# Performance work log

Hardware: AMD Instinct MI355X
Metric: run time of the kernel (lower is better)

Reference implementation:

```python
import jax, jax.numpy as jnp
import numpy as np

B, L, N, DM = 32, 12, 883, 64
DSP, DTP, H, HID, HOR = 128, 128, 4, 64, 12
E_SPA = 14128
ENC_LAYERS = 3
HIDDEN = 5 * HID  # 2*embed + node + tid + diw = 320


def _gat(x, es, et, W, a_s, a_d, bias, edge_att=None):
    # GATConv-style attention with optional per-edge info-bottleneck mask (gat_ib)
    n = x.shape[0]
    h = (x @ W).reshape(n, H, -1)            # [n,H,Dh]
    sc_s = (h * a_s).sum(-1)                 # [n,H]
    sc_d = (h * a_d).sum(-1)
    al = jax.nn.leaky_relu(sc_s[es] + sc_d[et], 0.2)   # [E,H]
    al = al - jax.ops.segment_max(al, et, num_segments=n)[et]
    ex = jnp.exp(al)
    a = ex / jax.ops.segment_sum(ex, et, num_segments=n)[et]
    if edge_att is not None:
        a = a * edge_att[:, None]
    out = jax.ops.segment_sum(a[..., None] * h[es], et, num_segments=n)
    return out.reshape(n, -1) + bias


def _gsat(x, ei, gat_p, ext_p):
    # GSAT: embed -> extractor MLP on edge endpoint pairs -> sigmoid edge att -> masked conv
    es, et = ei[0], ei[1]
    emb = _gat(x, es, et, *gat_p)
    w1, b1, w2, b2, w3, b3 = ext_p
    f = jnp.concatenate([emb[es], emb[et]], axis=-1)
    logit = (jax.nn.relu(jax.nn.relu(f @ w1 + b1) @ w2 + b2) @ w3 + b3)[:, 0]
    att = jax.nn.sigmoid(logit)  # eval-mode (no concrete-relaxation sampling)
    return _gat(x, es, et, *gat_p, edge_att=att)


def setup_inputs():
    key = jax.random.key(0)
    ks = iter(jax.random.split(key, 80))
    def nrm(shape, s=0.02):
        return jax.random.normal(next(ks), shape, jnp.float32) * s
    hist = jax.random.normal(next(ks), (B, L, N, 3), jnp.float32)
    tid = jax.random.randint(next(ks), (B, L, N), 0, 288).astype(jnp.float32)
    diw = jax.random.randint(next(ks), (B, L, N), 0, 7).astype(jnp.float32)
    hist = hist.at[..., 1].set(tid).at[..., 2].set(diw)
    ei_spa = jax.random.randint(next(ks), (2, E_SPA), 0, N).astype(jnp.int32)
    g = jnp.arange(L, dtype=jnp.int32)
    ei_temp = jnp.stack([jnp.repeat(g, L), jnp.tile(g, L)])  # dense lag x lag temporal graph
    inp = dict(history_data=hist, edge_idx_spa=ei_spa, edge_idx_temp=ei_temp)
    inp.update(
        node_emb=nrm((N, HID)), tid_emb=nrm((288, HID)), diw_emb=nrm((7, HID)),
        start_w=nrm((3, DM)), start_b=jnp.zeros((DM,), jnp.float32),
        ts_w=nrm((DM * L, HID)), ts_b=jnp.zeros((HID,), jnp.float32),
        tr_spat_w=nrm((L * DM, DSP)), tr_spat_b=jnp.zeros((DSP,), jnp.float32),
        inv_spat_w=nrm((DSP, L * DM)), inv_spat_b=jnp.zeros((L * DM,), jnp.float32),
        tr_temp_w=nrm((N * DM, DTP)), tr_temp_b=jnp.zeros((DTP,), jnp.float32),
        inv_temp_w=nrm((DTP, N * DM)), inv_temp_b=jnp.zeros((N * DM,), jnp.float32),
        gat_sp_w=nrm((DSP, DSP)), gat_sp_asrc=nrm((H, DSP // H)), gat_sp_adst=nrm((H, DSP // H)), gat_sp_bias=jnp.zeros((DSP,), jnp.float32),
        ext_sp_w1=nrm((2 * DSP, 4 * DSP)), ext_sp_b1=jnp.zeros((4 * DSP,), jnp.float32),
        ext_sp_w2=nrm((4 * DSP, DSP)), ext_sp_b2=jnp.zeros((DSP,), jnp.float32),
        ext_sp_w3=nrm((DSP, 1)), ext_sp_b3=jnp.zeros((1,), jnp.float32),
        gat_tp_w=nrm((DTP, DTP)), gat_tp_asrc=nrm((H, DTP // H)), gat_tp_adst=nrm((H, DTP // H)), gat_tp_bias=jnp.zeros((DTP,), jnp.float32),
        ext_tp_w1=nrm((2 * DTP, 4 * DTP)), ext_tp_b1=jnp.zeros((4 * DTP,), jnp.float32),
        ext_tp_w2=nrm((4 * DTP, DTP)), ext_tp_b2=jnp.zeros((DTP,), jnp.float32),
        ext_tp_w3=nrm((DTP, 1)), ext_tp_b3=jnp.zeros((1,), jnp.float32),
        enc_w1=nrm((ENC_LAYERS, HIDDEN, HIDDEN)), enc_b1=jnp.zeros((ENC_LAYERS, HIDDEN), jnp.float32),
        enc_w2=nrm((ENC_LAYERS, HIDDEN, HIDDEN)), enc_b2=jnp.zeros((ENC_LAYERS, HIDDEN), jnp.float32),
        reg_w=nrm((HIDDEN, HOR)), reg_b=jnp.zeros((HOR,), jnp.float32),
    )
    return inp


def reference(history_data, edge_idx_spa, edge_idx_temp, node_emb, tid_emb, diw_emb,
              start_w, start_b, ts_w, ts_b,
              tr_spat_w, tr_spat_b, inv_spat_w, inv_spat_b,
              tr_temp_w, tr_temp_b, inv_temp_w, inv_temp_b,
              gat_sp_w, gat_sp_asrc, gat_sp_adst, gat_sp_bias,
              ext_sp_w1, ext_sp_b1, ext_sp_w2, ext_sp_b2, ext_sp_w3, ext_sp_b3,
              gat_tp_w, gat_tp_asrc, gat_tp_adst, gat_tp_bias,
              ext_tp_w1, ext_tp_b1, ext_tp_w2, ext_tp_b2, ext_tp_w3, ext_tp_b3,
              enc_w1, enc_b1, enc_w2, enc_b2, reg_w, reg_b):
    b, l, n = history_data.shape[:3]
    tid = jax.lax.stop_gradient(history_data[:, -1, :, 1]).astype(jnp.int32)
    diw = jax.lax.stop_gradient(history_data[:, -1, :, 2]).astype(jnp.int32)
    X = history_data[..., :3] @ start_w + start_b           # [B,L,N,DM]
    res = X.transpose(0, 2, 1, 3).reshape(b, n, l * DM)      # [B,N,L*DM]
    ts_res = res @ ts_w + ts_b                               # conv1x1 over nodes == per-node linear
    gp_sp = (gat_sp_w, gat_sp_asrc, gat_sp_adst, gat_sp_bias)
    ep_sp = (ext_sp_w1, ext_sp_b1, ext_sp_w2, ext_sp_b2, ext_sp_w3, ext_sp_b3)
    gp_tp = (gat_tp_w, gat_tp_asrc, gat_tp_adst, gat_tp_bias)
    ep_tp = (ext_tp_w1, ext_tp_b1, ext_tp_w2, ext_tp_b2, ext_tp_w3, ext_tp_b3)
    # batch_st_gsat: per-sample spatial GSAT then temporal GSAT (vmapped instead of Python loop)
    spa_in = res @ tr_spat_w + tr_spat_b                     # [B,N,DSP]
    spa_out = jax.vmap(lambda xx: _gsat(xx, edge_idx_spa, gp_sp, ep_sp))(spa_in)
    spa_back = (spa_out @ inv_spat_w + inv_spat_b).reshape(b, n, l, DM).transpose(0, 2, 1, 3)
    temp_in = spa_back.reshape(b, l, n * DM) @ tr_temp_w + tr_temp_b   # [B,L,DTP]
    temp_out = jax.vmap(lambda xx: _gsat(xx, edge_idx_temp, gp_tp, ep_tp))(temp_in)
    temp_back = (temp_out @ inv_temp_w + inv_temp_b).reshape(b, l, n, DM)
    ts_temp = temp_back.transpose(0, 2, 1, 3).reshape(b, n, l * DM) @ ts_w + ts_b
    hid = jnp.concatenate([
        ts_res, ts_temp,
        jnp.broadcast_to(node_emb, (b, n, HID)),
        tid_emb[tid], diw_emb[diw],
    ], axis=-1)                                              # [B,N,320]
    for i in range(ENC_LAYERS):  # MLP_res: x + fc2(relu(fc1(x)))
        hid = hid + jax.nn.relu(hid @ enc_w1[i] + enc_b1[i]) @ enc_w2[i] + enc_b2[i]
    pred = hid @ reg_w + reg_b                               # [B,N,HOR]
    return pred.transpose(0, 2, 1)[..., None]                # [B,HOR,N,1]
```

## Files before the change

kernel.cpp:

```cpp
#include <hip/hip_runtime.h>
#include <hip/hip_bf16.h>
#include <cstdint>
#include <cstddef>

#define B_   32
#define L_   12
#define N_   883
#define DM_  64
#define E_SP 14128
#define E_TP 144
#define NT_  12
#define RBN  28256
#define RBL  384
#define LDM  768
#define NDM  56512

static inline int cdiv_h(int a, int b){ return (a+b-1)/b; }

__device__ __forceinline__ ushort f2bf(float f){
    unsigned u = __float_as_uint(f);
    unsigned lsb = (u >> 16) & 1u;
    u += 0x7fffu + lsb;
    return (ushort)(u >> 16);
}
__device__ __forceinline__ float bf2f(ushort h){
    return __uint_as_float(((unsigned)h) << 16);
}
__device__ __forceinline__ ushort f2h(float f){
    _Float16 h = (_Float16)f;
    ushort r; __builtin_memcpy(&r, &h, 2);
    return r;
}

typedef __bf16 bf16x8 __attribute__((ext_vector_type(8)));
typedef _Float16 f16x8 __attribute__((ext_vector_type(8)));
typedef _Float16 f16x2 __attribute__((ext_vector_type(2)));
typedef float  f32x4  __attribute__((ext_vector_type(4)));
typedef short  s16x2  __attribute__((ext_vector_type(2)));
union BF8 { bf16x8 v; ushort u[8]; unsigned w[4]; int4 i; };
union HF8 { f16x8 v; ushort u[8]; unsigned w[4]; int4 i; };

__device__ __forceinline__ unsigned pkrelu(unsigned x){
    s16x2 v;
    __builtin_memcpy(&v, &x, 4);
    s16x2 z = 0;
    v = __builtin_elementwise_max(v, z);
    unsigned r;
    __builtin_memcpy(&r, &v, 4);
    return r;
}
__device__ __forceinline__ unsigned pkaddh(unsigned x, unsigned y){
    f16x2 a, b;
    __builtin_memcpy(&a, &x, 4);
    __builtin_memcpy(&b, &y, 4);
    a = a + b;
    unsigned r;
    __builtin_memcpy(&r, &a, 4);
    return r;
}

__global__ void k_res(const float* __restrict__ hist, const float* __restrict__ sw,
                      const float* __restrict__ sb, ushort* __restrict__ resHi,
                      ushort* __restrict__ resLo)
{
    int idx = blockIdx.x*256 + threadIdx.x;
    if (idx >= RBN*LDM) return;
    int r = idx / LDM, col = idx - r*LDM;
    int b = r / N_, n = r - b*N_;
    int l = col >> 6, d = col & 63;
    const float* hp = hist + ((size_t)(b*L_ + l)*N_ + n)*3;
    float v = hp[0]*sw[d] + hp[1]*sw[64+d] + hp[2]*sw[128+d] + sb[d];
    ushort hi = f2bf(v);
    resHi[idx] = hi;
    resLo[idx] = f2bf(v - bf2f(hi));
}

template<int CT, int AMODE, int EPI, bool RELU, bool RES>
__launch_bounds__(256)
__global__ void mgemm(const ushort* __restrict__ A, const ushort* __restrict__ WT,
                      const float* __restrict__ bias, float* __restrict__ resF,
                      void* __restrict__ outP, int M, int N, int K)
{
    const int t = threadIdx.x, wv = t >> 6, l = t & 63;
    const int lr = l & 15, lk = l >> 4;
    const int row0 = blockIdx.y*64 + wv*16;
    const int col0 = blockIdx.x * (CT*16);
    int arr = row0 + lr; if (arr >= M) arr = M-1;
    int ab = 0, an = 0;
    if (AMODE == 1) { ab = arr / N_; an = arr - ab*N_; }
    const ushort* ap = A + (size_t)arr*K + lk*8;
    f32x4 acc[CT] = {};
    for (int k0 = 0; k0 < K; k0 += 32) {
        BF8 af;
        if (AMODE == 0) af.i = *(const int4*)(ap + k0);
        else {
            int k = k0 + lk*8; int ll = k >> 6, d = k & 63;
            af.i = *(const int4*)(A + ((size_t)(ab*L_ + ll))*NDM + (size_t)an*64 + d);
        }
        #pragma unroll
        for (int ct = 0; ct < CT; ++ct) {
            BF8 bf; bf.i = *(const int4*)&WT[(size_t)(col0 + ct*16 + lr)*K + k0 + lk*8];
            acc[ct] = __builtin_amdgcn_mfma_f32_16x16x32_bf16(af.v, bf.v, acc[ct], 0, 0, 0);
        }
    }
    #pragma unroll
    for (int ct = 0; ct < CT; ++ct) {
        int c = col0 + ct*16 + lr;
        float bv = 0.f;
        if (EPI == 2) { if (bias && c < 12) bv = bias[c]; }
        else if (bias) bv = bias[c];
        #pragma unroll
        for (int g = 0; g < 4; ++g) {
            int r = row0 + lk*4 + g;
            if (r >= M) continue;
            float v = acc[ct][g] + bv;
            if (RELU) v = fmaxf(v, 0.f);
            if (RES) {
                v += resF[(size_t)r*N + c];
                resF[(size_t)r*N + c] = v;
            }
            if (EPI == 0) {
                ((ushort*)outP)[(size_t)r*N + c] = f2bf(v);
            } else if (EPI == 1) {
                ((float*)outP)[(size_t)r*N + c] = v;
            } else if (EPI == 2) {
                if (c < 12) {
                    int b = r / N_, n = r - (r/N_)*N_;
                    ((float*)outP)[((size_t)(b*L_ + c))*N_ + n] = v;
                }
            } else {
                int b = r / N_, n = r - (r/N_)*N_;
                ((ushort*)outP)[((size_t)(b*L_ + (c>>6)))*NDM + (size_t)n*64 + (c&63)] = f2bf(v);
            }
        }
    }
}

template<int RT, int CT, int EPI, bool RELU, bool RES>
__launch_bounds__(256)
__global__ void mgemm_rt(const ushort* __restrict__ A, const ushort* __restrict__ WT,
                         const float* __restrict__ bias, float* __restrict__ resF,
                         void* __restrict__ outP, int M, int N, int K)
{
    const int t = threadIdx.x, wv = t >> 6, l = t & 63;
    const int lr = l & 15, lk = l >> 4;
    const int rowbase = blockIdx.y*(4*RT*16) + wv*(RT*16);
    const int col0 = blockIdx.x * (CT*16);
    const ushort* ap[RT];
    #pragma unroll
    for (int rt = 0; rt < RT; ++rt) {
        int arr = rowbase + rt*16 + lr; if (arr >= M) arr = M-1;
        ap[rt] = A + (size_t)arr*K + lk*8;
    }
    f32x4 acc[RT][CT] = {};
    for (int k0 = 0; k0 < K; k0 += 32) {
        BF8 af[RT];
        #pragma unroll
        for (int rt = 0; rt < RT; ++rt) af[rt].i = *(const int4*)(ap[rt] + k0);
        #pragma unroll
        for (int ct = 0; ct < CT; ++ct) {
            BF8 bf; bf.i = *(const int4*)&WT[(size_t)(col0 + ct*16 + lr)*K + k0 + lk*8];
            #pragma unroll
            for (int rt = 0; rt < RT; ++rt)
                acc[rt][ct] = __builtin_amdgcn_mfma_f32_16x16x32_bf16(af[rt].v, bf.v,
                                                                     acc[rt][ct], 0, 0, 0);
        }
    }
    #pragma unroll
    for (int rt = 0; rt < RT; ++rt)
        #pragma unroll
        for (int ct = 0; ct < CT; ++ct) {
            int c = col0 + ct*16 + lr;
            float bv = bias ? bias[c] : 0.f;
            #pragma unroll
            for (int g = 0; g < 4; ++g) {
                int r = rowbase + rt*16 + lk*4 + g;
                if (r >= M) continue;
                float v = acc[rt][ct][g] + bv;
                if (RELU) v = fmaxf(v, 0.f);
                if (RES) {
                    v += resF[(size_t)r*N + c];
                    resF[(size_t)r*N + c] = v;
                }
                if (EPI == 0) {
                    ((ushort*)outP)[(size_t)r*N + c] = f2bf(v);
                } else if (EPI == 1) {
                    ((float*)outP)[(size_t)r*N + c] = v;
                } else if (EPI == 4) {
                    ((ushort*)outP)[(size_t)r*N + c] = f2h(v);
                } else {
                    int b = r / N_, n = r - (r/N_)*N_;
                    ((ushort*)outP)[((size_t)(b*L_ + (c>>6)))*NDM + (size_t)n*64 + (c&63)] = f2bf(v);
                }
            }
        }
}

template<int CT>
__launch_bounds__(256)
__global__ void mgemm_hl(const ushort* __restrict__ Ahi, const ushort* __restrict__ Alo,
                         const ushort* __restrict__ WThi, const ushort* __restrict__ WTlo,
                         const float* __restrict__ bias, float* __restrict__ outF,
                         int M, int N, int K)
{
    const int t = threadIdx.x, wv = t >> 6, l = t & 63;
    const int lr = l & 15, lk = l >> 4;
    const int row0 = blockIdx.y*64 + wv*16;
    const int col0 = blockIdx.x * (CT*16);
    int arr = row0 + lr; if (arr >= M) arr = M-1;
    const ushort* aph = Ahi + (size_t)arr*K + lk*8;
    const ushort* apl = Alo + (size_t)arr*K + lk*8;
    f32x4 acc[CT] = {};
    for (int k0 = 0; k0 < K; k0 += 32) {
        BF8 ah, al_;
        ah.i  = *(const int4*)(aph + k0);
        al_.i = *(const int4*)(apl + k0);
        #pragma unroll
        for (int ct = 0; ct < CT; ++ct) {
            size_t wo = (size_t)(col0 + ct*16 + lr)*K + k0 + lk*8;
            BF8 bh, bl;
            bh.i = *(const int4*)&WThi[wo];
            bl.i = *(const int4*)&WTlo[wo];
            acc[ct] = __builtin_amdgcn_mfma_f32_16x16x32_bf16(ah.v,  bh.v, acc[ct], 0, 0, 0);
            acc[ct] = __builtin_amdgcn_mfma_f32_16x16x32_bf16(al_.v, bh.v, acc[ct], 0, 0, 0);
            acc[ct] = __builtin_amdgcn_mfma_f32_16x16x32_bf16(ah.v,  bl.v, acc[ct], 0, 0, 0);
        }
    }
    #pragma unroll
    for (int ct = 0; ct < CT; ++ct) {
        int c = col0 + ct*16 + lr;
        float bv = bias ? bias[c] : 0.f;
        #pragma unroll
        for (int g = 0; g < 4; ++g) {
            int r = row0 + lk*4 + g;
            if (r >= M) continue;
            outF[(size_t)r*N + c] = acc[ct][g] + bv;
        }
    }
}

#define TCH 1024
__launch_bounds__(256)
__global__ void temp_in_mfma(const ushort* __restrict__ AT, const ushort* __restrict__ WtT,
                             float* __restrict__ out)
{
    const int t = threadIdx.x, wv = t >> 6, l = t & 63;
    const int lr = l & 15, lk = l >> 4;
    const int row0 = blockIdx.y * 96;
    const int c0 = wv * 32;
    const int k0b = blockIdx.x * TCH;
    const int kend = (k0b + TCH < NDM) ? (k0b + TCH) : NDM;
    f32x4 acc[6][2] = {};
    for (int k0 = k0b; k0 < kend; k0 += 32) {
        BF8 b0, b1;
        b0.i = *(const int4*)&WtT[(size_t)(c0 + lr)*NDM + k0 + lk*8];
        b1.i = *(const int4*)&WtT[(size_t)(c0 + 16 + lr)*NDM + k0 + lk*8];
        #pragma unroll
        for (int m = 0; m < 6; ++m) {
            BF8 af; af.i = *(const int4*)&AT[(size_t)(row0 + m*16 + lr)*NDM + k0 + lk*8];
            acc[m][0] = __builtin_amdgcn_mfma_f32_16x16x32_bf16(af.v, b0.v, acc[m][0], 0, 0, 0);
            acc[m][1] = __builtin_amdgcn_mfma_f32_16x16x32_bf16(af.v, b1.v, acc[m][1], 0, 0, 0);
        }
    }
    #pragma unroll
    for (int m = 0; m < 6; ++m)
        #pragma unroll
        for (int ct = 0; ct < 2; ++ct) {
            int c = c0 + ct*16 + lr;
            #pragma unroll
            for (int g = 0; g < 4; ++g) {
                int r = row0 + m*16 + lk*4 + g;
                atomicAdd(&out[(size_t)r*128 + c], acc[m][ct][g]);
            }
        }
}

__global__ void k_sc(const ushort* __restrict__ h, const float* __restrict__ as_,
                     const float* __restrict__ ad_, float* __restrict__ scs,
                     float* __restrict__ scd, int R)
{
    int r = blockIdx.x*256 + threadIdx.x;
    if (r >= R) return;
    const ushort* hr = h + (size_t)r*128;
    #pragma unroll
    for (int hh = 0; hh < 4; ++hh) {
        float ss = 0.f, sd = 0.f;
        #pragma unroll
        for (int k = 0; k < 32; ++k) {
            float hv = bf2f(hr[hh*32 + k]);
            ss += hv*as_[hh*32+k];
            sd += hv*ad_[hh*32+k];
        }
        scs[(size_t)r*4+hh] = ss;
        scd[(size_t)r*4+hh] = sd;
    }
}

__global__ void k_attE(const float* __restrict__ scs, const float* __restrict__ scd,
                       const int* __restrict__ ei, int E, int NN,
                       float* __restrict__ a_buf, float* __restrict__ nsum)
{
    int idx = blockIdx.x*256 + threadIdx.x;
    if (idx >= B_*E) return;
    int b = idx / E, e = idx - b*E;
    int s = ei[e], tg = ei[E+e];
    const float* ps = scs + (size_t)(b*NN+s)*4;
    const float* pd = scd + (size_t)(b*NN+tg)*4;
    float* ns = nsum + (size_t)(b*NN+tg)*4;
    float* pa = a_buf + (size_t)idx*4;
    #pragma unroll
    for (int hh = 0; hh < 4; ++hh) {
        float al = ps[hh] + pd[hh];
        al = al > 0.f ? al : 0.2f*al;
        float ex = expf(al);
        pa[hh] = ex;
        atomicAdd(ns + hh, ex);
    }
}

__global__ void k_count(const int* __restrict__ ei, int E, int* __restrict__ counts){
    int e = blockIdx.x*256 + threadIdx.x;
    if (e < E) atomicAdd(&counts[ei[E + e]], 1);
}
__global__ void k_scan(const int* __restrict__ counts, int* __restrict__ off,
                       int* __restrict__ cur, int n)
{
    __shared__ int s[1024];
    int t = threadIdx.x;
    int v0 = (t < n) ? counts[t] : 0;
    s[t] = v0;
    __syncthreads();
    for (int o = 1; o < 1024; o <<= 1) {
        int v = (t >= o) ? s[t-o] : 0;
        __syncthreads();
        s[t] += v;
        __syncthreads();
    }
    if (t < n) {
        off[t+1] = s[t];
        cur[t] = s[t] - v0;
        if (t == 0) off[0] = 0;
    }
}
__global__ void k_fill(const int* __restrict__ ei, int E, int* __restrict__ cur,
                       int* __restrict__ lst){
    int e = blockIdx.x*256 + threadIdx.x;
    if (e < E) {
        int pos = atomicAdd(&cur[ei[E+e]], 1);
        lst[pos] = e;
    }
}

template<bool USE_ATT>
__global__ void k_gather(const ushort* __restrict__ h, const float* __restrict__ a_buf,
                         const float* __restrict__ nsum, const float* __restrict__ att,
                         const int* __restrict__ ei, const int* __restrict__ off,
                         const int* __restrict__ lst, const float* __restrict__ bias,
                         ushort* __restrict__ out, int E, int NN)
{
    int bn = blockIdx.x*4 + (threadIdx.x >> 6);
    int b = bn / NN, n = bn - b*NN;
    int lane = threadIdx.x & 63;
    int c0 = lane*2;
    int hh = lane >> 4;
    float rn = 1.f / nsum[(size_t)bn*4 + hh];
    int o0 = off[n], o1 = off[n+1];
    float ax = 0.f, ay = 0.f;
    for (int i = o0; i < o1; ++i) {
        int e = lst[i];
        float a = a_buf[((size_t)b*E + e)*4 + hh] * rn;
        if (USE_ATT) a *= att[(size_t)b*E + e];
        int s = ei[e];
        unsigned hv = *(const unsigned*)&h[((size_t)b*NN + s)*128 + c0];
        ax += a * __uint_as_float(hv << 16);
        ay += a * __uint_as_float(hv & 0xffff0000u);
    }
    ushort2 o2;
    o2.x = f2bf(ax + bias[c0]);
    o2.y = f2bf(ay + bias[c0+1]);
    *(ushort2*)&out[(size_t)bn*128 + c0] = o2;
}

__global__ void k_prepW2(const float* __restrict__ W2, ushort* __restrict__ W2T)
{
    int idx = blockIdx.x*256 + threadIdx.x;
    if (idx >= 512*128) return;
    int k = idx >> 7, c = idx & 127;
    W2T[(size_t)c*512 + k] = f2h(W2[idx]);
}
__global__ void k_prepT(const float* __restrict__ W, ushort* __restrict__ WT, int K, int N)
{
    int idx = blockIdx.x*256 + threadIdx.x;
    if (idx >= K*N) return;
    int k = idx / N, c = idx - k*N;
    WT[(size_t)c*K + k] = f2bf(W[idx]);
}
__global__ void k_prepT_hl(const float* __restrict__ W, ushort* __restrict__ WThi,
                           ushort* __restrict__ WTlo, int K, int N)
{
    int idx = blockIdx.x*256 + threadIdx.x;
    if (idx >= K*N) return;
    int k = idx / N, c = idx - k*N;
    float v = W[idx];
    ushort hi = f2bf(v);
    WThi[(size_t)c*K + k] = hi;
    WTlo[(size_t)c*K + k] = f2bf(v - bf2f(hi));
}
__global__ void k_prepWtT(const float* __restrict__ W, ushort* __restrict__ WT)
{
    __shared__ ushort tile[128][129];
    int k0 = blockIdx.x * 128;
    int t = threadIdx.x;
    for (int i = t; i < 128*128; i += 256) {
        int k = i >> 7, c = i & 127;
        int kk = k0 + k;
        tile[c][k] = (kk < NDM) ? f2bf(W[(size_t)kk*128 + c]) : (ushort)0;
    }
    __syncthreads();
    for (int i = t; i < 128*128; i += 256) {
        int c = i >> 7, k = i & 127;
        int kk = k0 + k;
        if (kk < NDM) WT[(size_t)c*NDM + kk] = tile[c][k];
    }
}
__global__ void k_prepT_big(const float* __restrict__ W, ushort* __restrict__ WT)
{
    __shared__ float tile[128][65];
    int c0 = blockIdx.x * 64;
    int t = threadIdx.x;
    for (int i = t; i < 128*64; i += 256) {
        int k = i >> 6, ci = i & 63;
        tile[k][ci] = W[(size_t)k*NDM + c0 + ci];
    }
    __syncthreads();
    for (int i = t; i < 64*128; i += 256) {
        int ci = i >> 7, k = i & 127;
        WT[(size_t)(c0 + ci)*128 + k] = f2bf(tile[k][ci]);
    }
}
__global__ void k_bcat(const float* __restrict__ b1, float* __restrict__ dst){
    int i = blockIdx.x*256 + threadIdx.x;
    if (i < 1024) dst[i] = (i < 512) ? b1[i] : 0.f;
}

template<bool SWZ>
__launch_bounds__(256, 3)
__global__ void ext2_mfma(const ushort* __restrict__ PQ, const ushort* __restrict__ W2T,
                          const float* __restrict__ b2, const float* __restrict__ w3,
                          const float* __restrict__ b3p, const int* __restrict__ ei,
                          const int* __restrict__ lst,
                          float* __restrict__ att, int E, int NN, int nblk)
{
    __shared__ ushort Bs[2][128*40];
    int bid = blockIdx.x;
    if (SWZ) {
        bid = (blockIdx.x & 7) * (gridDim.x >> 3) + (blockIdx.x >> 3);
        if (bid >= nblk) bid = nblk - 1;
    }
    const int t = threadIdx.x;
    const int wv = t >> 6, l = t & 63;
    const int lr = l & 15, lk = l >> 4;

    const ushort* pr[2]; const ushort* qr[2];
    int row0[2];
    #pragma unroll
    for (int rt = 0; rt < 2; ++rt) {
        row0[rt] = bid*128 + wv*32 + rt*16;
        int r = row0[rt] + lr;
        int b = (int)((unsigned)r / (unsigned)E), i = r - b*E;
        int e = lst[i];
        pr[rt] = PQ + ((size_t)b*NN + ei[e])*1024 + lk*8;
        qr[rt] = PQ + ((size_t)b*NN + ei[E+e])*1024 + 512 + lk*8;
    }
    const int sc = t >> 1, sh = (t & 1) * 16;
    const ushort* wsrc = W2T + (size_t)sc*512 + sh;
    ushort* wd0 = &Bs[0][sc*40 + sh];
    ushort* wd1 = &Bs[1][sc*40 + sh];

    {
        int4 a0 = *(const int4*)(wsrc);
        int4 a1 = *(const int4*)(wsrc + 8);
        *(int4*)wd0 = a0;
        *(int4*)(wd0 + 8) = a1;
    }
    HF8 pu[2], qu[2];
    #pragma unroll
    for (int rt = 0; rt < 2; ++rt) {
        pu[rt].i = *(const int4*)(pr[rt]);
        qu[rt].i = *(const int4*)(qr[rt]);
    }
    int4 bnA = *(const int4*)(wsrc + 32);
    int4 bnB = *(const int4*)(wsrc + 40);
    __syncthreads();

    f32x4 acc[2][8] = {};
    for (int kc = 0; kc < 16; ++kc) {
        const int cb = kc & 1;
        HF8 af[2];
        #pragma unroll
        for (int rt = 0; rt < 2; ++rt)
            #pragma unroll
            for (int j = 0; j < 4; ++j)
                af[rt].w[j] = pkrelu(pkaddh(pu[rt].w[j], qu[rt].w[j]));
        {
            int ka = (kc+1 < 15) ? kc+1 : 15;
            #pragma unroll
            for (int rt = 0; rt < 2; ++rt) {
                pu[rt].i = *(const int4*)(pr[rt] + ka*32);
                qu[rt].i = *(const int4*)(qr[rt] + ka*32);
            }
        }
        __builtin_amdgcn_s_setprio(1);
        #pragma unroll
        for (int ct = 0; ct < 8; ++ct) {
            HF8 bfm;
            bfm.v = *(const f16x8*)&Bs[cb][(ct*16 + lr)*40 + lk*8];
            #pragma unroll
            for (int rt = 0; rt < 2; ++rt)
                acc[rt][ct] = __builtin_amdgcn_mfma_f32_16x16x32_f16(af[rt].v, bfm.v,
                                                                    acc[rt][ct], 0, 0, 0);
        }
        __builtin_amdgcn_s_setprio(0);
        if (kc < 15) {
            ushort* wd = cb ? wd0 : wd1;
            *(int4*)wd = bnA;
            *(int4*)(wd + 8) = bnB;
        }
        {
            int kb = (kc+2 < 15) ? kc+2 : 15;
            bnA = *(const int4*)(wsrc + kb*32);
            bnB = *(const int4*)(wsrc + kb*32 + 8);
        }
        __syncthreads();
    }
    float b3 = b3p[0];
    #pragma unroll
    for (int rt = 0; rt < 2; ++rt) {
        float part[4] = {0.f,0.f,0.f,0.f};
        #pragma unroll
        for (int ct = 0; ct < 8; ++ct) {
            int c = ct*16 + lr;
            float b2v = b2[c], w3v = w3[c];
            #pragma unroll
            for (int g = 0; g < 4; ++g)
                part[g] += fmaxf(acc[rt][ct][g] + b2v, 0.f) * w3v;
        }
        #pragma unroll
        for (int m = 1; m < 16; m <<= 1)
            #pragma unroll
            for (int g = 0; g < 4; ++g)
                part[g] += __shfl_xor(part[g], m, 64);
        if (lr == 0) {
            #pragma unroll
            for (int g = 0; g < 4; ++g) {
                int rr = row0[rt] + lk*4 + g;
                int b = (int)((unsigned)rr / (unsigned)E), i = rr - b*E;
                int e = lst[i];
                att[(size_t)b*E + e] = 1.f/(1.f + expf(-(part[g] + b3)));
            }
        }
    }
}

__global__ void k_bias_fill(float* __restrict__ dst, const float* __restrict__ bias, int n){
    int i = blockIdx.x*256 + threadIdx.x;
    if (i < n) dst[i] = bias[i & 127];
}
__global__ void k_f2b(const float* __restrict__ src, ushort* __restrict__ dst, int n){
    int i = blockIdx.x*256 + threadIdx.x;
    if (i < n) dst[i] = f2bf(src[i]);
}

__global__ void k_hid(const float* __restrict__ ts_res, const float* __restrict__ ts_temp,
                      const float* __restrict__ node_emb, const float* __restrict__ tid_emb,
                      const float* __restrict__ diw_emb, const float* __restrict__ hist,
                      float* __restrict__ hid, ushort* __restrict__ hidB)
{
    int idx = blockIdx.x*256 + threadIdx.x;
    if (idx >= RBN*320) return;
    int r = idx / 320, c = idx - r*320;
    int b = r / N_, n = r - b*N_;
    float v;
    if (c < 64)        v = ts_res[(size_t)r*64 + c];
    else if (c < 128)  v = ts_temp[(size_t)r*64 + (c-64)];
    else if (c < 192)  v = node_emb[(size_t)n*64 + (c-128)];
    else if (c < 256) {
        int tid = (int)hist[((size_t)(b*L_ + (L_-1))*N_ + n)*3 + 1];
        v = tid_emb[(size_t)tid*64 + (c-192)];
    } else {
        int diw = (int)hist[((size_t)(b*L_ + (L_-1))*N_ + n)*3 + 2];
        v = diw_emb[(size_t)diw*64 + (c-256)];
    }
    hid[idx] = v;
    hidB[idx] = f2bf(v);
}

extern "C" void kernel_launch(void* const* d_in, const int* in_sizes, int n_in,
                              void* d_out, int out_size, void* d_ws, size_t ws_size,
                              hipStream_t stream)
{
    (void)in_sizes; (void)n_in; (void)out_size; (void)ws_size;
    const float* hist      = (const float*)d_in[0];
    const int*   ei_sp     = (const int*)  d_in[1];
    const int*   ei_tp     = (const int*)  d_in[2];
    const float* node_emb  = (const float*)d_in[3];
    const float* tid_emb   = (const float*)d_in[4];
    const float* diw_emb   = (const float*)d_in[5];
    const float* start_w   = (const float*)d_in[6];
    const float* start_b   = (const float*)d_in[7];
    const float* ts_w      = (const float*)d_in[8];
    const float* ts_b      = (const float*)d_in[9];
    const float* tr_spat_w = (const float*)d_in[10];
    const float* tr_spat_b = (const float*)d_in[11];
    const float* inv_spat_w= (const float*)d_in[12];
    const float* inv_spat_b= (const float*)d_in[13];
    const float* tr_temp_w = (const float*)d_in[14];
    const float* tr_temp_b = (const float*)d_in[15];
    const float* inv_temp_w= (const float*)d_in[16];
    const float* inv_temp_b= (const float*)d_in[17];
    const float* gat_sp_w  = (const float*)d_in[18];
    const float* gat_sp_as = (const float*)d_in[19];
    const float* gat_sp_ad = (const float*)d_in[20];
    const float* gat_sp_b  = (const float*)d_in[21];
    const float* ext_sp_w1 = (const float*)d_in[22];
    const float* ext_sp_b1 = (const float*)d_in[23];
    const float* ext_sp_w2 = (const float*)d_in[24];
    const float* ext_sp_b2 = (const float*)d_in[25];
    const float* ext_sp_w3 = (const float*)d_in[26];
    const float* ext_sp_b3 = (const float*)d_in[27];
    const float* gat_tp_w  = (const float*)d_in[28];
    const float* gat_tp_as = (const float*)d_in[29];
    const float* gat_tp_ad = (const float*)d_in[30];
    const float* gat_tp_b  = (const float*)d_in[31];
    const float* ext_tp_w1 = (const float*)d_in[32];
    const float* ext_tp_b1 = (const float*)d_in[33];
    const float* ext_tp_w2 = (const float*)d_in[34];
    const float* ext_tp_b2 = (const float*)d_in[35];
    const float* ext_tp_w3 = (const float*)d_in[36];
    const float* ext_tp_b3 = (const float*)d_in[37];
    const float* enc_w1    = (const float*)d_in[38];
    const float* enc_b1    = (const float*)d_in[39];
    const float* enc_w2    = (const float*)d_in[40];
    const float* enc_b2    = (const float*)d_in[41];
    const float* reg_w     = (const float*)d_in[42];
    const float* reg_b     = (const float*)d_in[43];
    float* out = (float*)d_out;

    size_t o = 0;
    char* wsb = (char*)d_ws;
    auto allocB = [&](size_t bytes) -> void* {
        void* p = wsb + o;
        o += (bytes + 255) & ~(size_t)255;
        return p;
    };
    void* bufA = allocB((size_t)RBN*768*2);
    void* bufB = allocB((size_t)RBN*768*2);
    void* bufC = allocB((size_t)RBN*512*2);
    void* bufD = allocB((size_t)RBN*320*2);
    float*  ts_res  = (float*)allocB((size_t)RBN*64*4);
    ushort* spaB    = (ushort*)allocB((size_t)RBN*128*2);
    ushort* hB      = (ushort*)allocB((size_t)RBN*128*2);
    float*  sc_s    = (float*)allocB((size_t)RBN*4*4);
    float*  sc_d    = (float*)allocB((size_t)RBN*4*4);
    float*  nsum    = (float*)allocB((size_t)RBN*4*4);
    float*  a_buf   = (float*)allocB((size_t)B_*E_SP*4*4);
    float*  att     = (float*)allocB((size_t)B_*E_SP*4);
    ushort* embB    = (ushort*)allocB((size_t)RBN*128*2);
    int*    csr     = (int*)allocB(17024*4);
    float*  temp_in = (float*)allocB((size_t)RBL*128*4);
    ushort* tempB   = (ushort*)allocB((size_t)RBL*128*2);
    ushort* toutB   = (ushort*)allocB((size_t)RBL*128*2);
    ushort* PQ_t    = (ushort*)allocB((size_t)RBL*1024*2);
    float*  ts_temp = (float*)allocB((size_t)RBN*64*4);
    ushort* W2T_sp  = (ushort*)allocB(512*128*2);
    ushort* W2T_tp  = (ushort*)allocB(512*128*2);
    ushort* WtT     = (ushort*)allocB((size_t)128*NDM*2);
    ushort* itWT    = (ushort*)allocB((size_t)NDM*128*2);
    ushort* tspWT   = (ushort*)allocB(128*768*2);
    ushort* ispWT   = (ushort*)allocB(768*128*2);
    ushort* gspWT   = (ushort*)allocB(128*128*2);
    ushort* gtpWT   = (ushort*)allocB(128*128*2);
    ushort* w1catT_sp = (ushort*)allocB((size_t)1024*128*2);
    ushort* w1catT_tp = (ushort*)allocB((size_t)1024*128*2);
    float*  b1cat_sp  = (float*)allocB(1024*4);
    float*  b1cat_tp  = (float*)allocB(1024*4);
    ushort* w1T_enc = (ushort*)allocB((size_t)3*320*320*2);
    ushort* w2T_enc = (ushort*)allocB((size_t)3*320*320*2);
    ushort* tswT_hi = (ushort*)allocB(64*768*2);
    ushort* tswT_lo = (ushort*)allocB(64*768*2);
    ushort* reg_wT  = (ushort*)allocB(16*320*2);

    ushort* resHi = (ushort*)bufA;
    ushort* resLo = (ushort*)bufB;
    ushort* AT    = (ushort*)bufA;
    float*  hid   = (float*)bufA;
    ushort* PQ_sp = (ushort*)bufB;
    ushort* tback = (ushort*)bufB;
    ushort* hidB  = (ushort*)bufC;
    ushort* R1b   = (ushort*)bufD;

    int* counts_sp = csr;
    int* off_sp    = csr + 883;
    int* cur_sp    = csr + 1767;
    int* list_sp   = csr + 2650;
    int* counts_tp = csr + 16778;
    int* off_tp    = csr + 16790;
    int* cur_tp    = csr + 16803;
    int* list_tp   = csr + 16815;

    hipMemsetAsync(counts_sp, 0, 883*4, stream);
    k_count<<<cdiv_h(E_SP,256),256,0,stream>>>(ei_sp, E_SP, counts_sp);
    k_scan<<<1,1024,0,stream>>>(counts_sp, off_sp, cur_sp, 883);
    k_fill<<<cdiv_h(E_SP,256),256,0,stream>>>(ei_sp, E_SP, cur_sp, list_sp);
    hipMemsetAsync(counts_tp, 0, 12*4, stream);
    k_count<<<1,256,0,stream>>>(ei_tp, E_TP, counts_tp);
    k_scan<<<1,1024,0,stream>>>(counts_tp, off_tp, cur_tp, 12);
    k_fill<<<1,256,0,stream>>>(ei_tp, E_TP, cur_tp, list_tp);
    k_prepW2<<<cdiv_h(512*128,256),256,0,stream>>>(ext_sp_w2, W2T_sp);
    k_prepW2<<<cdiv_h(512*128,256),256,0,stream>>>(ext_tp_w2, W2T_tp);
    k_prepWtT<<<cdiv_h(NDM,128),256,0,stream>>>(tr_temp_w, WtT);
    k_prepT_big<<<NDM/64,256,0,stream>>>(inv_temp_w, itWT);
    k_prepT<<<cdiv_h(768*128,256),256,0,stream>>>(tr_spat_w, tspWT, 768, 128);
    k_prepT<<<cdiv_h(128*768,256),256,0,stream>>>(inv_spat_w, ispWT, 128, 768);
    k_prepT<<<cdiv_h(128*128,256),256,0,stream>>>(gat_sp_w, gspWT, 128, 128);
    k_prepT<<<cdiv_h(128*128,256),256,0,stream>>>(gat_tp_w, gtpWT, 128, 128);
    k_prepT<<<cdiv_h(128*512,256),256,0,stream>>>(ext_sp_w1,           w1catT_sp,           128, 512);
    k_prepT<<<cdiv_h(128*512,256),256,0,stream>>>(ext_sp_w1 + 128*512, w1catT_sp + 512*128, 128, 512);
    k_prepT<<<cdiv_h(128*512,256),256,0,stream>>>(ext_tp_w1,           w1catT_tp,           128, 512);
    k_prepT<<<cdiv_h(128*512,256),256,0,stream>>>(ext_tp_w1 + 128*512, w1catT_tp + 512*128, 128, 512);
    k_bcat<<<4,256,0,stream>>>(ext_sp_b1, b1cat_sp);
    k_bcat<<<4,256,0,stream>>>(ext_tp_b1, b1cat_tp);
    for (int i = 0; i < 3; ++i) {
        k_prepT<<<cdiv_h(320*320,256),256,0,stream>>>(enc_w1 + (size_t)i*320*320, w1T_enc + (size_t)i*320*320, 320, 320);
        k_prepT<<<cdiv_h(320*320,256),256,0,stream>>>(enc_w2 + (size_t)i*320*320, w2T_enc + (size_t)i*320*320, 320, 320);
    }
    k_prepT_hl<<<cdiv_h(768*64,256),256,0,stream>>>(ts_w, tswT_hi, tswT_lo, 768, 64);
    hipMemsetAsync(reg_wT, 0, 16*320*2, stream);
    k_prepT<<<cdiv_h(320*12,256),256,0,stream>>>(reg_w, reg_wT, 320, 12);

    k_res<<<cdiv_h(RBN*LDM,256),256,0,stream>>>(hist, start_w, start_b, resHi, resLo);
    mgemm_hl<4><<<dim3(1,442),256,0,stream>>>(resHi, resLo, tswT_hi, tswT_lo, ts_b, ts_res,
                                              RBN, 64, LDM);
    mgemm_rt<2,4,0,false,false><<<dim3(2,221),256,0,stream>>>(resHi, tspWT, tr_spat_b, nullptr,
                                                              spaB, RBN, 128, LDM);

    mgemm_rt<2,4,0,false,false><<<dim3(2,221),256,0,stream>>>(spaB, gspWT, nullptr, nullptr,
                                                              hB, RBN, 128, 128);
    k_sc<<<cdiv_h(RBN,256),256,0,stream>>>(hB, gat_sp_as, gat_sp_ad, sc_s, sc_d, RBN);
    hipMemsetAsync(nsum, 0, (size_t)RBN*4*4, stream);
    k_attE<<<cdiv_h(B_*E_SP,256),256,0,stream>>>(sc_s, sc_d, ei_sp, E_SP, N_, a_buf, nsum);
    k_gather<false><<<RBN/4,256,0,stream>>>(hB, a_buf, nsum, nullptr, ei_sp, off_sp, list_sp,
                                            gat_sp_b, embB, E_SP, N_);
    mgemm_rt<2,8,4,false,false><<<dim3(8,221),256,0,stream>>>(embB, w1catT_sp, b1cat_sp, nullptr,
                                                              PQ_sp, RBN, 1024, 128);
    ext2_mfma<true><<<3536,256,0,stream>>>(PQ_sp, W2T_sp, ext_sp_b2, ext_sp_w3, ext_sp_b3,
                                           ei_sp, list_sp, att, E_SP, N_, (B_*E_SP)/128);
    k_gather<true><<<RBN/4,256,0,stream>>>(hB, a_buf, nsum, att, ei_sp, off_sp, list_sp,
                                           gat_sp_b, spaB, E_SP, N_);

    mgemm_rt<2,4,3,false,false><<<dim3(12,221),256,0,stream>>>(spaB, ispWT, inv_spat_b, nullptr,
                                                               AT, RBN, 768, 128);
    k_bias_fill<<<cdiv_h(RBL*128,256),256,0,stream>>>(temp_in, tr_temp_b, RBL*128);
    temp_in_mfma<<<dim3(56,4),256,0,stream>>>(AT, WtT, temp_in);
    k_f2b<<<cdiv_h(RBL*128,256),256,0,stream>>>(temp_in, tempB, RBL*128);

    mgemm_rt<2,4,0,false,false><<<dim3(2,3),256,0,stream>>>(tempB, gtpWT, nullptr, nullptr,
                                                            hB, RBL, 128, 128);
    k_sc<<<cdiv_h(RBL,256),256,0,stream>>>(hB, gat_tp_as, gat_tp_ad, sc_s, sc_d, RBL);
    hipMemsetAsync(nsum, 0, (size_t)RBL*4*4, stream);
    k_attE<<<cdiv_h(B_*E_TP,256),256,0,stream>>>(sc_s, sc_d, ei_tp, E_TP, NT_, a_buf, nsum);
    k_gather<false><<<RBL/4,256,0,stream>>>(hB, a_buf, nsum, nullptr, ei_tp, off_tp, list_tp,
                                            gat_tp_b, embB, E_TP, NT_);
    mgemm_rt<2,8,4,false,false><<<dim3(8,3),256,0,stream>>>(embB, w1catT_tp, b1cat_tp, nullptr,
                                                            PQ_t, RBL, 1024, 128);
    ext2_mfma<false><<<(B_*E_TP)/128,256,0,stream>>>(PQ_t, W2T_tp, ext_tp_b2, ext_tp_w3,
                                                     ext_tp_b3, ei_tp, list_tp, att, E_TP, NT_,
                                                     (B_*E_TP)/128);
    k_gather<true><<<RBL/4,256,0,stream>>>(hB, a_buf, nsum, att, ei_tp, off_tp, list_tp,
                                           gat_tp_b, toutB, E_TP, NT_);

    mgemm_rt<2,4,0,false,false><<<dim3(883,3),256,0,stream>>>(toutB, itWT, inv_temp_b, nullptr,
                                                              tback, RBL, NDM, 128);
    mgemm<4,1,1,false,false><<<dim3(1,442),256,0,stream>>>(tback, tswT_hi, ts_b, nullptr,
                                                           ts_temp, RBN, 64, LDM);

    k_hid<<<cdiv_h(RBN*320,256),256,0,stream>>>(ts_res, ts_temp, node_emb, tid_emb, diw_emb, hist,
                                                hid, hidB);
    for (int i = 0; i < 3; ++i) {
        mgemm_rt<2,5,0,true,false><<<dim3(4,221),256,0,stream>>>(hidB, w1T_enc + (size_t)i*320*320,
                                                                 enc_b1 + i*320, nullptr, R1b, RBN, 320, 320);
        mgemm_rt<2,5,0,false,true><<<dim3(4,221),256,0,stream>>>(R1b, w2T_enc + (size_t)i*320*320,
                                                                 enc_b2 + i*320, hid, hidB, RBN, 320, 320);
    }
    mgemm<1,0,2,false,false><<<dim3(1,442),256,0,stream>>>(hidB, reg_wT, reg_b, nullptr,
                                                           out, RBN, 16, 320);
}
```

Measured before the change: 1.407 ms.

## Fuse edge softmax into CSR gather and double-buffer ext2 operand prefetch

Removes the separate edge-attention kernel, its atomics, the memset and the a_buf/nsum buffers. Each gather lane now recomputes leaky-relu and exp per incoming edge and accumulates the softmax denominator locally, normalising at the end. This drops atomic traffic and a full edge-sized buffer round trip, at the cost of redundant exp work across the 16 lanes of each head and across the two gather passes. Separately, the ext2 MFMA loop is unrolled by two, with A and B register sets so the endpoint-feature loads are prefetched two steps ahead with static LDS buffer indices.

Result: faster. 1.323 ms (-6.0%).

```diff
diff --git a/kernel.cpp b/kernel.cpp
--- a/kernel.cpp
+++ b/kernel.cpp
@@ -296,28 +296,6 @@
     }
 }
 
-__global__ void k_attE(const float* __restrict__ scs, const float* __restrict__ scd,
-                       const int* __restrict__ ei, int E, int NN,
-                       float* __restrict__ a_buf, float* __restrict__ nsum)
-{
-    int idx = blockIdx.x*256 + threadIdx.x;
-    if (idx >= B_*E) return;
-    int b = idx / E, e = idx - b*E;
-    int s = ei[e], tg = ei[E+e];
-    const float* ps = scs + (size_t)(b*NN+s)*4;
-    const float* pd = scd + (size_t)(b*NN+tg)*4;
-    float* ns = nsum + (size_t)(b*NN+tg)*4;
-    float* pa = a_buf + (size_t)idx*4;
-    #pragma unroll
-    for (int hh = 0; hh < 4; ++hh) {
-        float al = ps[hh] + pd[hh];
-        al = al > 0.f ? al : 0.2f*al;
-        float ex = expf(al);
-        pa[hh] = ex;
-        atomicAdd(ns + hh, ex);
-    }
-}
-
 __global__ void k_count(const int* __restrict__ ei, int E, int* __restrict__ counts){
     int e = blockIdx.x*256 + threadIdx.x;
     if (e < E) atomicAdd(&counts[ei[E + e]], 1);
@@ -352,8 +330,8 @@
 }
 
 template<bool USE_ATT>
-__global__ void k_gather(const ushort* __restrict__ h, const float* __restrict__ a_buf,
-                         const float* __restrict__ nsum, const float* __restrict__ att,
+__global__ void k_gather(const ushort* __restrict__ h, const float* __restrict__ scs,
+                         const float* __restrict__ scd, const float* __restrict__ att,
                          const int* __restrict__ ei, const int* __restrict__ off,
                          const int* __restrict__ lst, const float* __restrict__ bias,
                          ushort* __restrict__ out, int E, int NN)
@@ -363,21 +341,25 @@
     int lane = threadIdx.x & 63;
     int c0 = lane*2;
     int hh = lane >> 4;
-    float rn = 1.f / nsum[(size_t)bn*4 + hh];
+    float sd = scd[(size_t)bn*4 + hh];
     int o0 = off[n], o1 = off[n+1];
-    float ax = 0.f, ay = 0.f;
+    float ax = 0.f, ay = 0.f, sa = 0.f;
     for (int i = o0; i < o1; ++i) {
         int e = lst[i];
-        float a = a_buf[((size_t)b*E + e)*4 + hh] * rn;
-        if (USE_ATT) a *= att[(size_t)b*E + e];
         int s = ei[e];
+        float al = scs[(size_t)(b*NN + s)*4 + hh] + sd;
+        al = al > 0.f ? al : 0.2f*al;
+        float ex = expf(al);
+        sa += ex;
+        float a = USE_ATT ? ex * att[(size_t)b*E + e] : ex;
         unsigned hv = *(const unsigned*)&h[((size_t)b*NN + s)*128 + c0];
         ax += a * __uint_as_float(hv << 16);
         ay += a * __uint_as_float(hv & 0xffff0000u);
     }
+    float rn = (sa > 0.f) ? 1.f/sa : 0.f;
     ushort2 o2;
-    o2.x = f2bf(ax + bias[c0]);
-    o2.y = f2bf(ay + bias[c0+1]);
+    o2.x = f2bf(ax*rn + bias[c0]);
+    o2.y = f2bf(ay*rn + bias[c0+1]);
     *(ushort2*)&out[(size_t)bn*128 + c0] = o2;
 }
 
@@ -477,61 +459,93 @@
     ushort* wd0 = &Bs[0][sc*40 + sh];
     ushort* wd1 = &Bs[1][sc*40 + sh];
 
-    {
-        int4 a0 = *(const int4*)(wsrc);
-        int4 a1 = *(const int4*)(wsrc + 8);
-        *(int4*)wd0 = a0;
-        *(int4*)(wd0 + 8) = a1;
-    }
-    HF8 pu[2], qu[2];
+    HF8 puA[2], quA[2], puB[2], quB[2];
     #pragma unroll
     for (int rt = 0; rt < 2; ++rt) {
-        pu[rt].i = *(const int4*)(pr[rt]);
-        qu[rt].i = *(const int4*)(qr[rt]);
+        puA[rt].i = *(const int4*)(pr[rt]);
+        quA[rt].i = *(const int4*)(qr[rt]);
+    }
+    int4 a0 = *(const int4*)(wsrc);
+    int4 a1 = *(const int4*)(wsrc + 8);
+    #pragma unroll
+    for (int rt = 0; rt < 2; ++rt) {
+        puB[rt].i = *(const int4*)(pr[rt] + 32);
+        quB[rt].i = *(const int4*)(qr[rt] + 32);
     }
     int4 bnA = *(const int4*)(wsrc + 32);
     int4 bnB = *(const int4*)(wsrc + 40);
+    *(int4*)wd0 = a0;
+    *(int4*)(wd0 + 8) = a1;
     __syncthreads();
 
     f32x4 acc[2][8] = {};
-    for (int kc = 0; kc < 16; ++kc) {
-        const int cb = kc & 1;
-        HF8 af[2];
-        #pragma unroll
-        for (int rt = 0; rt < 2; ++rt)
-            #pragma unroll
-            for (int j = 0; j < 4; ++j)
-                af[rt].w[j] = pkrelu(pkaddh(pu[rt].w[j], qu[rt].w[j]));
+    for (int kc2 = 0; kc2 < 16; kc2 += 2) {
         {
-            int ka = (kc+1 < 15) ? kc+1 : 15;
-            #pragma unroll
-            for (int rt = 0; rt < 2; ++rt) {
-                pu[rt].i = *(const int4*)(pr[rt] + ka*32);
-                qu[rt].i = *(const int4*)(qr[rt] + ka*32);
-            }
-        }
-        __builtin_amdgcn_s_setprio(1);
-        #pragma unroll
-        for (int ct = 0; ct < 8; ++ct) {
-            HF8 bfm;
-            bfm.v = *(const f16x8*)&Bs[cb][(ct*16 + lr)*40 + lk*8];
+            HF8 af[2];
             #pragma unroll
             for (int rt = 0; rt < 2; ++rt)
-                acc[rt][ct] = __builtin_amdgcn_mfma_f32_16x16x32_f16(af[rt].v, bfm.v,
-                                                                    acc[rt][ct], 0, 0, 0);
-        }
-        __builtin_amdgcn_s_setprio(0);
-        if (kc < 15) {
-            ushort* wd = cb ? wd0 : wd1;
-            *(int4*)wd = bnA;
-            *(int4*)(wd + 8) = bnB;
-        }
-        {
-            int kb = (kc+2 < 15) ? kc+2 : 15;
+                #pragma unroll
+                for (int j = 0; j < 4; ++j)
+                    af[rt].w[j] = pkrelu(pkaddh(puA[rt].w[j], quA[rt].w[j]));
+            if (kc2 < 14) {
+                #pragma unroll
+                for (int rt = 0; rt < 2; ++rt) {
+                    puA[rt].i = *(const int4*)(pr[rt] + (kc2+2)*32);
+                    quA[rt].i = *(const int4*)(qr[rt] + (kc2+2)*32);
+                }
+            }
+            __builtin_amdgcn_s_setprio(1);
+            #pragma unroll
+            for (int ct = 0; ct < 8; ++ct) {
+                HF8 bfm;
+                bfm.v = *(const f16x8*)&Bs[0][(ct*16 + lr)*40 + lk*8];
+                #pragma unroll
+                for (int rt = 0; rt < 2; ++rt)
+                    acc[rt][ct] = __builtin_amdgcn_mfma_f32_16x16x32_f16(af[rt].v, bfm.v,
+                                                                        acc[rt][ct], 0, 0, 0);
+            }
+            __builtin_amdgcn_s_setprio(0);
+            *(int4*)wd1 = bnA;
+            *(int4*)(wd1 + 8) = bnB;
+            int kb = (kc2+2 < 15) ? kc2+2 : 15;
             bnA = *(const int4*)(wsrc + kb*32);
             bnB = *(const int4*)(wsrc + kb*32 + 8);
-        }
-        __syncthreads();
+            __syncthreads();
+        }
+        {
+            HF8 af[2];
+            #pragma unroll
+            for (int rt = 0; rt < 2; ++rt)
+                #pragma unroll
+                for (int j = 0; j < 4; ++j)
+                    af[rt].w[j] = pkrelu(pkaddh(puB[rt].w[j], quB[rt].w[j]));
+            if (kc2 < 14) {
+                #pragma unroll
+                for (int rt = 0; rt < 2; ++rt) {
+                    puB[rt].i = *(const int4*)(pr[rt] + (kc2+3)*32);
+                    quB[rt].i = *(const int4*)(qr[rt] + (kc2+3)*32);
+                }
+            }
+            __builtin_amdgcn_s_setprio(1);
+            #pragma unroll
+            for (int ct = 0; ct < 8; ++ct) {
+                HF8 bfm;
+                bfm.v = *(const f16x8*)&Bs[1][(ct*16 + lr)*40 + lk*8];
+                #pragma unroll
+                for (int rt = 0; rt < 2; ++rt)
+                    acc[rt][ct] = __builtin_amdgcn_mfma_f32_16x16x32_f16(af[rt].v, bfm.v,
+                                                                        acc[rt][ct], 0, 0, 0);
+            }
+            __builtin_amdgcn_s_setprio(0);
+            if (kc2 < 14) {
+                *(int4*)wd0 = bnA;
+                *(int4*)(wd0 + 8) = bnB;
+            }
+            int kb = (kc2+3 < 15) ? kc2+3 : 15;
+            bnA = *(const int4*)(wsrc + kb*32);
+            bnB = *(const int4*)(wsrc + kb*32 + 8);
+            __syncthreads();
+        }
     }
     float b3 = b3p[0];
     #pragma unroll
@@ -662,8 +676,6 @@
     ushort* hB      = (ushort*)allocB((size_t)RBN*128*2);
     float*  sc_s    = (float*)allocB((size_t)RBN*4*4);
     float*  sc_d    = (float*)allocB((size_t)RBN*4*4);
-    float*  nsum    = (float*)allocB((size_t)RBN*4*4);
-    float*  a_buf   = (float*)allocB((size_t)B_*E_SP*4*4);
     float*  att     = (float*)allocB((size_t)B_*E_SP*4);
     ushort* embB    = (ushort*)allocB((size_t)RBN*128*2);
     int*    csr     = (int*)allocB(17024*4);
@@ -747,15 +759,13 @@
     mgemm_rt<2,4,0,false,false><<<dim3(2,221),256,0,stream>>>(spaB, gspWT, nullptr, nullptr,
                                                               hB, RBN, 128, 128);
     k_sc<<<cdiv_h(RBN,256),256,0,stream>>>(hB, gat_sp_as, gat_sp_ad, sc_s, sc_d, RBN);
-    hipMemsetAsync(nsum, 0, (size_t)RBN*4*4, stream);
-    k_attE<<<cdiv_h(B_*E_SP,256),256,0,stream>>>(sc_s, sc_d, ei_sp, E_SP, N_, a_buf, nsum);
-    k_gather<false><<<RBN/4,256,0,stream>>>(hB, a_buf, nsum, nullptr, ei_sp, off_sp, list_sp,
+    k_gather<false><<<RBN/4,256,0,stream>>>(hB, sc_s, sc_d, nullptr, ei_sp, off_sp, list_sp,
                                             gat_sp_b, embB, E_SP, N_);
     mgemm_rt<2,8,4,false,false><<<dim3(8,221),256,0,stream>>>(embB, w1catT_sp, b1cat_sp, nullptr,
                                                               PQ_sp, RBN, 1024, 128);
     ext2_mfma<true><<<3536,256,0,stream>>>(PQ_sp, W2T_sp, ext_sp_b2, ext_sp_w3, ext_sp_b3,
                                            ei_sp, list_sp, att, E_SP, N_, (B_*E_SP)/128);
-    k_gather<true><<<RBN/4,256,0,stream>>>(hB, a_buf, nsum, att, ei_sp, off_sp, list_sp,
+    k_gather<true><<<RBN/4,256,0,stream>>>(hB, sc_s, sc_d, att, ei_sp, off_sp, list_sp,
                                            gat_sp_b, spaB, E_SP, N_);
 
     mgemm_rt<2,4,3,false,false><<<dim3(12,221),256,0,stream>>>(spaB, ispWT, inv_spat_b, nullptr,
@@ -767,16 +777,14 @@
     mgemm_rt<2,4,0,false,false><<<dim3(2,3),256,0,stream>>>(tempB, gtpWT, nullptr, nullptr,
                                                             hB, RBL, 128, 128);
     k_sc<<<cdiv_h(RBL,256),256,0,stream>>>(hB, gat_tp_as, gat_tp_ad, sc_s, sc_d, RBL);
-    hipMemsetAsync(nsum, 0, (size_t)RBL*4*4, stream);
-    k_attE<<<cdiv_h(B_*E_TP,256),256,0,stream>>>(sc_s, sc_d, ei_tp, E_TP, NT_, a_buf, nsum);
-    k_gather<false><<<RBL/4,256,0,stream>>>(hB, a_buf, nsum, nullptr, ei_tp, off_tp, list_tp,
+    k_gather<false><<<RBL/4,256,0,stream>>>(hB, sc_s, sc_d, nullptr, ei_tp, off_tp, list_tp,
                                             gat_tp_b, embB, E_TP, NT_);
     mgemm_rt<2,8,4,false,false><<<dim3(8,3),256,0,stream>>>(embB, w1catT_tp, b1cat_tp, nullptr,
                                                             PQ_t, RBL, 1024, 128);
     ext2_mfma<false><<<(B_*E_TP)/128,256,0,stream>>>(PQ_t, W2T_tp, ext_tp_b2, ext_tp_w3,
                                                      ext_tp_b3, ei_tp, list_tp, att, E_TP, NT_,
                                                      (B_*E_TP)/128);
-    k_gather<true><<<RBL/4,256,0,stream>>>(hB, a_buf, nsum, att, ei_tp, off_tp, list_tp,
+    k_gather<true><<<RBL/4,256,0,stream>>>(hB, sc_s, sc_d, att, ei_tp, off_tp, list_tp,
                                            gat_tp_b, toutB, E_TP, NT_);
 
     mgemm_rt<2,4,0,false,false><<<dim3(883,3),256,0,stream>>>(toutB, itWT, inv_temp_b, nullptr,
```
